# Optimization experiments

Measured on AMD Instinct MI355X. Metric: run time of the kernel, lower is better.

The kernel has to match this reference:

```python
import jax, jax.numpy as jnp
import numpy as np
import math

N = 8192
D_IN = 512
LOCAL_D = 512
GLOBAL_D = 512


def setup_inputs() -> dict:
    key = jax.random.key(0)
    ks = jax.random.split(key, 16)
    s = 1.0 / math.sqrt(D_IN)
    adj = jax.random.bernoulli(ks[0], 0.01, (N, N))
    adj = adj | jnp.eye(N, dtype=bool)
    return {
        "adj_matrix": adj,
        "x": jax.random.normal(ks[1], (N, D_IN), jnp.float32),
        "masked_x": jax.random.normal(ks[2], (N, D_IN), jnp.float32),
        # weights stored as [in, out] so y = x @ W (+ b)
        "Wlq": jax.random.normal(ks[3], (D_IN, LOCAL_D), jnp.float32) * s,
        "Wlk": jax.random.normal(ks[4], (D_IN, LOCAL_D), jnp.float32) * s,
        "Wlv": jax.random.normal(ks[5], (D_IN, D_IN), jnp.float32) * s,
        "blv": jax.random.normal(ks[6], (D_IN,), jnp.float32) * 0.01,
        "Wgq": jax.random.normal(ks[7], (D_IN, GLOBAL_D), jnp.float32) * s,
        "Wgk": jax.random.normal(ks[8], (D_IN, GLOBAL_D), jnp.float32) * s,
        "Wgv": jax.random.normal(ks[9], (D_IN, D_IN), jnp.float32) * s,
        "bgv": jax.random.normal(ks[10], (D_IN,), jnp.float32) * 0.01,
        "Wes": jax.random.normal(ks[11], (D_IN, 1), jnp.float32) * s,
        "Wev": jax.random.normal(ks[12], (D_IN, D_IN), jnp.float32) * s,
        "bev": jax.random.normal(ks[13], (D_IN,), jnp.float32) * 0.01,
    }


def reference(adj_matrix, x, masked_x, Wlq, Wlk, Wlv, blv, Wgq, Wgk, Wgv, bgv, Wes, Wev, bev):
    scale = 1.0 / math.sqrt(D_IN)  # note: original scales by sqrt(d_in), not sqrt(local_d)
    x_bar = jnp.mean(x, axis=0, keepdims=True)            # [1, d_in]

    lQ = masked_x @ Wlq                                   # [N, local_d]
    lK = x @ Wlk                                          # [N, local_d]
    lV = x @ Wlv + blv                                    # [N, d_out]
    gQ = masked_x @ Wgq                                   # [N, global_d]
    gK = x_bar @ Wgk                                      # [1, global_d]
    gV = x_bar @ Wgv + bgv                                # [1, d_out]
    es = masked_x @ Wes                                   # [N, 1]
    eV = masked_x @ Wev + bev                             # [N, d_out]

    local_scores = (lQ @ lK.T) * scale                    # [N, N]
    local_scores = jnp.where(adj_matrix, local_scores, jnp.float32(-1e9))
    global_scores = (gQ @ gK.T) * scale                   # [N, 1]

    # joint stable softmax across local row + global scalar + essential scalar
    max_score = jnp.maximum(jnp.max(local_scores, axis=1, keepdims=True),
                            jnp.maximum(global_scores, es))  # [N, 1]
    le = jnp.exp(local_scores - max_score)                # [N, N]
    ge = jnp.exp(global_scores - max_score)               # [N, 1]
    ee = jnp.exp(es - max_score)                          # [N, 1]
    denom = jnp.sum(le, axis=-1, keepdims=True) + ge + ee # [N, 1]

    res = (le / denom) @ lV + (ge / denom) * gV + (ee / denom) * eV  # [N, d_out]
    x_recon = jnp.maximum(res, masked_x)
    return x_recon
```

## Files before the change

kernel.cpp:

```cpp
#include <hip/hip_runtime.h>

typedef unsigned short u16;
typedef unsigned int   u32;
typedef unsigned char  u8;
typedef __attribute__((ext_vector_type(8))) short bf16x8;
typedef __attribute__((ext_vector_type(4))) float f32x4;

#define DEV __device__ __forceinline__

static constexpr float SCALE = 0.044194173824159216f;
static constexpr float MFIX  = 8.0f;

DEV u16 f2bf(float f) {
  u32 u = __float_as_uint(f);
  u32 r = (u + 0x7fffu + ((u >> 16) & 1u)) >> 16;
  return (u16)r;
}
DEV float bf2f(u16 v) { u32 u = (u32)v << 16; return __uint_as_float(u); }

DEV void gl_lds16(const void* g, void* l) {
  __builtin_amdgcn_global_load_lds(
      (__attribute__((address_space(1))) void*)(void*)g,
      (__attribute__((address_space(3))) void*)l, 16, 0, 0);
}

__global__ void k_convert(const float* __restrict__ x, const float* __restrict__ mx,
                          u16* __restrict__ xbf, u16* __restrict__ mxbf) {
  const u32 stride = gridDim.x * blockDim.x;
  for (u32 idx = blockIdx.x * blockDim.x + threadIdx.x; idx < 2u * 1048576u; idx += stride) {
    const u32 t = idx >> 20;
    const u32 i = idx & 1048575u;
    const float4 v = t ? ((const float4*)mx)[i] : ((const float4*)x)[i];
    ushort4 o;
    o.x = f2bf(v.x); o.y = f2bf(v.y); o.z = f2bf(v.z); o.w = f2bf(v.w);
    ((ushort4*)(t ? mxbf : xbf))[i] = o;
  }
}

struct WtransJobs { const float* src[4]; u16* dst[4]; };

__global__ void k_wtrans(WtransJobs jobs) {
  __shared__ float tile[32][33];
  const int j  = blockIdx.z;
  const float* src = jobs.src[j];
  u16* dst = jobs.dst[j];
  const int o0 = blockIdx.x * 32;
  const int k0 = blockIdx.y * 32;
  const int tx = threadIdx.x, ty = threadIdx.y;
#pragma unroll
  for (int yy = 0; yy < 4; ++yy)
    tile[ty + yy * 8][tx] = src[(size_t)(k0 + ty + yy * 8) * 512 + (o0 + tx)];
  __syncthreads();
#pragma unroll
  for (int yy = 0; yy < 4; ++yy)
    dst[(size_t)(o0 + ty + yy * 8) * 512 + (k0 + tx)] = f2bf(tile[tx][ty + yy * 8]);
}

__global__ void k_adjdetect(const u8* __restrict__ adj, u32* __restrict__ flag) {
  u32 cnt = 0;
  const u32 stride = gridDim.x * blockDim.x;
  for (u32 i = blockIdx.x * blockDim.x + threadIdx.x; i < (1u << 22); i += stride)
    if ((i & 3u) && adj[i]) cnt++;
#pragma unroll
  for (int m = 1; m <= 32; m <<= 1) cnt += __shfl_xor(cnt, m);
  if ((threadIdx.x & 63) == 0 && cnt) atomicAdd(flag, cnt);
}

__global__ void k_adjbits(const u8* __restrict__ adj, const u32* __restrict__ flag,
                          u32* __restrict__ adjb) {
  const int row = blockIdx.x;
  const int w = threadIdx.x;
  u32 res = 0;
  if (*flag > 100u) {
    const uint4* p = (const uint4*)(adj + (size_t)row * 8192 + w * 32);
#pragma unroll
    for (int i = 0; i < 2; ++i) {
      const uint4 q = p[i];
      const u32 vs[4] = {q.x, q.y, q.z, q.w};
#pragma unroll
      for (int jj = 0; jj < 4; ++jj) {
        const u32 v = vs[jj];
        const int base = i * 16 + jj * 4;
        res |= ((v & 0x000000FFu) ? 1u : 0u) << (base + 0);
        res |= ((v & 0x0000FF00u) ? 1u : 0u) << (base + 1);
        res |= ((v & 0x00FF0000u) ? 1u : 0u) << (base + 2);
        res |= ((v & 0xFF000000u) ? 1u : 0u) << (base + 3);
      }
    }
  } else {
    const uint4* p = (const uint4*)((const u32*)adj + (size_t)row * 8192 + w * 32);
#pragma unroll
    for (int i = 0; i < 8; ++i) {
      const uint4 q = p[i];
      res |= (q.x ? 1u : 0u) << (i * 4 + 0);
      res |= (q.y ? 1u : 0u) << (i * 4 + 1);
      res |= (q.z ? 1u : 0u) << (i * 4 + 2);
      res |= (q.w ? 1u : 0u) << (i * 4 + 3);
    }
  }
  adjb[(size_t)row * 256 + w] = res;
}

__global__ void k_colsum(const float* __restrict__ x, float* __restrict__ part) {
  const int c = threadIdx.x;
  const int b = blockIdx.x;
  const int r0 = b * 128;
  float s = 0.f;
  for (int r = 0; r < 128; ++r) s += x[(size_t)(r0 + r) * 512 + c];
  part[b * 512 + c] = s;
}

__global__ void k_colsum2(const float* __restrict__ part, float* __restrict__ xbar) {
  const int c = threadIdx.x;
  float s = 0.f;
  for (int b = 0; b < 64; ++b) s += part[b * 512 + c];
  xbar[c] = s * (1.0f / 8192.0f);
}

__global__ void k_gproj(const float* __restrict__ xbar, const float* __restrict__ Wgk,
                        const float* __restrict__ Wgv, const float* __restrict__ bgv,
                        float* __restrict__ gK, float* __restrict__ gV) {
  const int o = threadIdx.x;
  if (blockIdx.x == 0) {
    float s = 0.f;
    for (int k = 0; k < 512; ++k) s += xbar[k] * Wgk[(size_t)k * 512 + o];
    gK[o] = s;
  } else {
    float s = bgv[o];
    for (int k = 0; k < 512; ++k) s += xbar[k] * Wgv[(size_t)k * 512 + o];
    gV[o] = s;
  }
}

__global__ void k_wcomb(const float* __restrict__ Wgq, const float* __restrict__ gK,
                        float* __restrict__ wcomb) {
  const int w = threadIdx.x >> 6, l = threadIdx.x & 63;
  const int k = blockIdx.x * 4 + w;
  float s = 0.f;
  for (int o = l; o < 512; o += 64) s += Wgq[(size_t)k * 512 + o] * gK[o];
#pragma unroll
  for (int m = 1; m <= 32; m <<= 1) s += __shfl_xor(s, m);
  if (l == 0) wcomb[k] = s;
}

__global__ void k_esgsc(const float* __restrict__ mx, const float* __restrict__ Wes,
                        const float* __restrict__ wcomb, float* __restrict__ es,
                        float* __restrict__ gsc) {
  const int w = threadIdx.x >> 6, l = threadIdx.x & 63;
  const int row = blockIdx.x * 4 + w;
  float se = 0.f, sg = 0.f;
  for (int k = l; k < 512; k += 64) {
    const float v = mx[(size_t)row * 512 + k];
    se += v * Wes[k];
    sg += v * wcomb[k];
  }
#pragma unroll
  for (int m = 1; m <= 32; m <<= 1) { se += __shfl_xor(se, m); sg += __shfl_xor(sg, m); }
  if (l == 0) { es[row] = se; gsc[row] = sg * SCALE; }
}

struct GemmOuts { u16* obf[2]; float* of32[2]; const float* bias[2]; };

__global__ __launch_bounds__(256) void k_gemm(const u16* __restrict__ A,
                                              const u16* __restrict__ BT, GemmOuts outs) {
  __shared__ char lds[16384];
  char* ldsA = lds;
  char* ldsB = lds + 8192;
  const int tid = threadIdx.x;
  const int w = tid >> 6, l = tid & 63, g = l >> 4, ln = l & 15;
  const int wr = w >> 1, wc = w & 1;
  const int bm0 = blockIdx.x * 128, bn0 = blockIdx.y * 128;
  f32x4 acc[4][4] = {};
  for (int kt = 0; kt < 16; ++kt) {
    const int k0 = kt * 32;
    __syncthreads();
#pragma unroll
    for (int it = 0; it < 2; ++it) {
      const int i = it * 256 + tid;
      const int o = i * 16;
      const int row = o >> 6;
      const int pos = (o ^ (((o >> 7) & 3) << 4)) & 63;
      const int ldso = (it * 256 + w * 64) * 16;
      gl_lds16((const char*)A + ((size_t)(bm0 + row) * 512 + k0) * 2 + pos, ldsA + ldso);
      gl_lds16((const char*)BT + ((size_t)(bn0 + row) * 512 + k0) * 2 + pos, ldsB + ldso);
    }
    __syncthreads();
    bf16x8 a[4], b[4];
#pragma unroll
    for (int i = 0; i < 4; ++i) {
      const int r = wr * 64 + i * 16 + ln;
      int off = r * 64 + g * 16; off ^= ((r >> 1) & 3) << 4;
      a[i] = *(const bf16x8*)(ldsA + off);
    }
#pragma unroll
    for (int j = 0; j < 4; ++j) {
      const int r = wc * 64 + j * 16 + ln;
      int off = r * 64 + g * 16; off ^= ((r >> 1) & 3) << 4;
      b[j] = *(const bf16x8*)(ldsB + off);
    }
#pragma unroll
    for (int i = 0; i < 4; ++i)
#pragma unroll
      for (int j = 0; j < 4; ++j)
        acc[i][j] = __builtin_amdgcn_mfma_f32_16x16x32_bf16(a[i], b[j], acc[i][j], 0, 0, 0);
  }
#pragma unroll
  for (int j = 0; j < 4; ++j) {
    const int gcol = bn0 + wc * 64 + j * 16 + ln;
    const int seg = gcol >> 9, c = gcol & 511;
    const float bias = outs.bias[seg] ? outs.bias[seg][c] : 0.f;
#pragma unroll
    for (int i = 0; i < 4; ++i) {
#pragma unroll
      for (int r = 0; r < 4; ++r) {
        const int grow = bm0 + wr * 64 + i * 16 + g * 4 + r;
        const float v = acc[i][j][r] + bias;
        if (outs.of32[seg]) outs.of32[seg][(size_t)grow * 512 + c] = v;
        else                outs.obf[seg][(size_t)grow * 512 + c] = f2bf(v);
      }
    }
  }
}

__global__ void k_vtrans(const u16* __restrict__ lV, u16* __restrict__ lVT) {
  __shared__ u16 tile[32][33];
  const int c0 = blockIdx.x * 32;
  const int r0 = blockIdx.y * 32;
  const int tx = threadIdx.x, ty = threadIdx.y;
#pragma unroll
  for (int yy = 0; yy < 4; ++yy)
    tile[ty + yy * 8][tx] = lV[(size_t)(r0 + ty + yy * 8) * 512 + (c0 + tx)];
  __syncthreads();
#pragma unroll
  for (int yy = 0; yy < 4; ++yy)
    lVT[(size_t)(c0 + ty + yy * 8) * 8192 + (r0 + tx)] = tile[tx][ty + yy * 8];
}

__global__ __launch_bounds__(256, 2) void k_attn(
    const u16* __restrict__ lQ, const u16* __restrict__ lK, const u16* __restrict__ lVT,
    const u32* __restrict__ adjb, u16* __restrict__ Opart, float* __restrict__ lpart) {
  __shared__ char lds[69632];
  char* ldsK = lds;
  char* ldsVT = lds + 32768;
  const int tid = threadIdx.x;
  const int w = tid >> 6, l = tid & 63, g = l >> 4, ln = l & 15;
  const int qg = w >> 1, dh = w & 1;
  char* ldsP = lds + 65536 + qg * 1024;
  const int bid = blockIdx.x;
  const int split = (bid & 7) >> 1;
  const int rblk = ((bid >> 3) << 1) | (bid & 1);
  const int rbase = rblk * 32 + qg * 16;

  bf16x8 q[16];
#pragma unroll
  for (int kk = 0; kk < 16; ++kk)
    q[kk] = *(const bf16x8*)(lQ + (size_t)(rbase + ln) * 512 + kk * 32 + g * 8);

  f32x4 acc[16] = {};
  float rl = 0.f;

  for (int ct = 0; ct < 64; ++ct) {
    const int c0 = split * 2048 + ct * 32;
    __syncthreads();
#pragma unroll
    for (int it = 0; it < 8; ++it) {
      const int o = (it * 256 + tid) * 16;
      const int row = o >> 10;
      const int pos = (o ^ ((row & 7) << 4)) & 1023;
      gl_lds16((const char*)lK + (size_t)(c0 + row) * 1024 + pos,
               ldsK + (it * 256 + w * 64) * 16);
    }
#pragma unroll
    for (int it = 0; it < 8; ++it) {
      const int o = (it * 256 + tid) * 16;
      const int row = o >> 6;
      const int pos = (o ^ (((o >> 7) & 3) << 4)) & 63;
      gl_lds16((const char*)lVT + (size_t)row * 16384 + (size_t)c0 * 2 + pos,
               ldsVT + (it * 256 + w * 64) * 16);
    }
    __syncthreads();

    const u32 wd = adjb[(size_t)(rbase + ln) * 256 + (c0 >> 5)];

    f32x4 s = {};
    {
      const int ra = dh * 16 + ln;
      const int sw = (ra & 7) << 4;
      __builtin_amdgcn_s_setprio(1);
#pragma unroll
      for (int kk = 0; kk < 16; ++kk) {
        const int off = (ra * 1024 + kk * 64 + g * 16) ^ sw;
        const bf16x8 kf = *(const bf16x8*)(ldsK + off);
        s = __builtin_amdgcn_mfma_f32_16x16x32_bf16(kf, q[kk], s, 0, 0, 0);
      }
      __builtin_amdgcn_s_setprio(0);
    }

    float p[4];
#pragma unroll
    for (int r = 0; r < 4; ++r) {
      const int kc = dh * 16 + g * 4 + r;
      p[r] = ((wd >> kc) & 1) ? __expf(s[r] * SCALE - MFIX) : 0.f;
      rl += p[r];
    }

    {
      const int sw = ((ln >> 1) & 3) << 4;
      ushort4 w0;
      w0.x = f2bf(p[0]); w0.y = f2bf(p[1]); w0.z = f2bf(p[2]); w0.w = f2bf(p[3]);
      *(ushort4*)(ldsP + ((ln * 64 + dh * 32 + g * 8) ^ sw)) = w0;
    }
    __syncthreads();

    const bf16x8 pa = *(const bf16x8*)(ldsP + ((ln * 64 + g * 16) ^ (((ln >> 1) & 3) << 4)));
    __builtin_amdgcn_s_setprio(1);
#pragma unroll
    for (int t = 0; t < 16; ++t) {
      const int r = (dh * 16 + t) * 16 + ln;
      int off = r * 64 + g * 16; off ^= ((r >> 1) & 3) << 4;
      const bf16x8 vf = *(const bf16x8*)(ldsVT + off);
      acc[t] = __builtin_amdgcn_mfma_f32_16x16x32_bf16(pa, vf, acc[t], 0, 0, 0);
    }
    __builtin_amdgcn_s_setprio(0);
  }

#pragma unroll
  for (int t = 0; t < 16; ++t)
#pragma unroll
    for (int i = 0; i < 4; ++i)
      Opart[((size_t)split * 8192 + rbase + g * 4 + i) * 512 + dh * 256 + t * 16 + ln] =
          f2bf(acc[t][i]);
  rl += __shfl_xor(rl, 16);
  rl += __shfl_xor(rl, 32);
  if (l < 16) lpart[((size_t)split * 2 + dh) * 8192 + rbase + l] = rl;
}

__global__ void k_combine(const u16* __restrict__ Opart, const float* __restrict__ lpart,
                          const float* __restrict__ gsc, const float* __restrict__ es,
                          const float* __restrict__ gV, const float* __restrict__ eV,
                          const float* __restrict__ mx, float* __restrict__ out) {
  const int row = blockIdx.x;
  const int tid = threadIdx.x;
  const float gs = gsc[row], e = es[row];
  const float M = fmaxf(MFIX, fmaxf(gs, e));
  const float eg = __expf(gs - M), ee = __expf(e - M);
  const float fL = __expf(MFIX - M);
  float lsum = 0.f;
#pragma unroll
  for (int s = 0; s < 8; ++s) lsum += lpart[(size_t)s * 8192 + row];
  const float inv = 1.f / (eg + ee + fL * lsum);
  for (int d = tid; d < 512; d += 256) {
    float o = 0.f;
#pragma unroll
    for (int s = 0; s < 4; ++s)
      o += bf2f(Opart[((size_t)s * 8192 + row) * 512 + d]);
    o = o * fL + eg * gV[d] + ee * eV[(size_t)row * 512 + d];
    out[(size_t)row * 512 + d] = fmaxf(o * inv, mx[(size_t)row * 512 + d]);
  }
}

static constexpr size_t OFF_XBF   = 0;
static constexpr size_t OFF_MXBF  = OFF_XBF   + (size_t)8192 * 512 * 2;
static constexpr size_t OFF_WMT   = OFF_MXBF  + (size_t)8192 * 512 * 2;
static constexpr size_t OFF_WXT   = OFF_WMT   + (size_t)1024 * 512 * 2;
static constexpr size_t OFF_LQ    = OFF_WXT   + (size_t)1024 * 512 * 2;
static constexpr size_t OFF_LK    = OFF_LQ    + (size_t)8192 * 512 * 2;
static constexpr size_t OFF_LV    = OFF_LK    + (size_t)8192 * 512 * 2;
static constexpr size_t OFF_LVT   = OFF_LV    + (size_t)8192 * 512 * 2;
static constexpr size_t OFF_EV    = OFF_LVT   + (size_t)8192 * 512 * 2;
static constexpr size_t OFF_ADJB  = OFF_EV    + (size_t)8192 * 512 * 4;
static constexpr size_t OFF_COLP  = OFF_ADJB  + (size_t)8192 * 256 * 4;
static constexpr size_t OFF_XBAR  = OFF_COLP  + (size_t)64 * 512 * 4;
static constexpr size_t OFF_GK    = OFF_XBAR  + 2048;
static constexpr size_t OFF_GV    = OFF_GK    + 2048;
static constexpr size_t OFF_WCOMB = OFF_GV    + 2048;
static constexpr size_t OFF_ES    = OFF_WCOMB + 2048;
static constexpr size_t OFF_GSC   = OFF_ES    + (size_t)8192 * 4;
static constexpr size_t OFF_OPART = OFF_GSC   + (size_t)8192 * 4;
static constexpr size_t OFF_LPART = OFF_OPART + (size_t)4 * 8192 * 512 * 2;
static constexpr size_t OFF_FLAG  = OFF_LPART + (size_t)8 * 8192 * 4;
static constexpr size_t WS_NEEDED = OFF_FLAG  + 64;

extern "C" void kernel_launch(void* const* d_in, const int* in_sizes, int n_in,
                              void* d_out, int out_size, void* d_ws, size_t ws_size,
                              hipStream_t stream) {
  const u8*    adj = (const u8*)d_in[0];
  const float* x   = (const float*)d_in[1];
  const float* mx  = (const float*)d_in[2];
  const float* Wlq = (const float*)d_in[3];
  const float* Wlk = (const float*)d_in[4];
  const float* Wlv = (const float*)d_in[5];
  const float* blv = (const float*)d_in[6];
  const float* Wgq = (const float*)d_in[7];
  const float* Wgk = (const float*)d_in[8];
  const float* Wgv = (const float*)d_in[9];
  const float* bgv = (const float*)d_in[10];
  const float* Wes = (const float*)d_in[11];
  const float* Wev = (const float*)d_in[12];
  const float* bev = (const float*)d_in[13];
  float* out = (float*)d_out;

  if (ws_size < WS_NEEDED) return;

  char* ws = (char*)d_ws;
  u16*   x_bf   = (u16*)(ws + OFF_XBF);
  u16*   mx_bf  = (u16*)(ws + OFF_MXBF);
  u16*   WmT    = (u16*)(ws + OFF_WMT);
  u16*   WxT    = (u16*)(ws + OFF_WXT);
  u16*   lQ     = (u16*)(ws + OFF_LQ);
  u16*   lK     = (u16*)(ws + OFF_LK);
  u16*   lV     = (u16*)(ws + OFF_LV);
  u16*   lVT    = (u16*)(ws + OFF_LVT);
  float* eV     = (float*)(ws + OFF_EV);
  u32*   adjb   = (u32*)(ws + OFF_ADJB);
  float* colp   = (float*)(ws + OFF_COLP);
  float* xbar   = (float*)(ws + OFF_XBAR);
  float* gK     = (float*)(ws + OFF_GK);
  float* gV     = (float*)(ws + OFF_GV);
  float* wcomb  = (float*)(ws + OFF_WCOMB);
  float* es     = (float*)(ws + OFF_ES);
  float* gsc    = (float*)(ws + OFF_GSC);
  u16*   Opart  = (u16*)(ws + OFF_OPART);
  float* lpart  = (float*)(ws + OFF_LPART);
  u32*   flag   = (u32*)(ws + OFF_FLAG);

  hipMemsetAsync(flag, 0, 4, stream);
  k_adjdetect<<<1024, 256, 0, stream>>>(adj, flag);

  k_convert<<<2048, 256, 0, stream>>>(x, mx, x_bf, mx_bf);

  WtransJobs wj;
  wj.src[0] = Wlq; wj.dst[0] = WmT;
  wj.src[1] = Wev; wj.dst[1] = WmT + (size_t)512 * 512;
  wj.src[2] = Wlk; wj.dst[2] = WxT;
  wj.src[3] = Wlv; wj.dst[3] = WxT + (size_t)512 * 512;
  k_wtrans<<<dim3(16, 16, 4), dim3(32, 8), 0, stream>>>(wj);

  k_adjbits<<<8192, 256, 0, stream>>>(adj, flag, adjb);
  k_colsum<<<64, 512, 0, stream>>>(x, colp);
  k_colsum2<<<1, 512, 0, stream>>>(colp, xbar);
  k_gproj<<<2, 512, 0, stream>>>(xbar, Wgk, Wgv, bgv, gK, gV);
  k_wcomb<<<128, 256, 0, stream>>>(Wgq, gK, wcomb);
  k_esgsc<<<2048, 256, 0, stream>>>(mx, Wes, wcomb, es, gsc);

  GemmOuts o1;
  o1.obf[0] = lQ;      o1.of32[0] = nullptr; o1.bias[0] = nullptr;
  o1.obf[1] = nullptr; o1.of32[1] = eV;      o1.bias[1] = bev;
  k_gemm<<<dim3(64, 8), 256, 0, stream>>>(mx_bf, WmT, o1);

  GemmOuts o2;
  o2.obf[0] = lK; o2.of32[0] = nullptr; o2.bias[0] = nullptr;
  o2.obf[1] = lV; o2.of32[1] = nullptr; o2.bias[1] = blv;
  k_gemm<<<dim3(64, 8), 256, 0, stream>>>(x_bf, WxT, o2);

  k_vtrans<<<dim3(16, 256), dim3(32, 8), 0, stream>>>(lV, lVT);
  k_attn<<<dim3(1024), 256, 0, stream>>>(lQ, lK, lVT, adjb, Opart, lpart);
  k_combine<<<8192, 256, 0, stream>>>(Opart, lpart, gsc, es, gV, eV, mx, out);
}
```

Before: 453.9 us.

## Merge two projection GEMMs into one launch and share V fragments across query groups

The two projection GEMM launches are combined into one grid, with blockIdx.y selecting the job, so the launch gap goes away and the GPU stays fuller. In the attention kernel each wave now reads P for both 16-row query groups and computes 8 output column tiles for both, instead of 16 column tiles for one group. This halves the V-fragment LDS reads per MFMA. It costs an extra P read per wave and changes the accumulator layout and output indexing.

Result: no change. 455.0 us (+0.2%).

```diff
diff --git a/kernel.cpp b/kernel.cpp
--- a/kernel.cpp
+++ b/kernel.cpp
@@ -161,15 +161,21 @@
 
 struct GemmOuts { u16* obf[2]; float* of32[2]; const float* bias[2]; };
 
-__global__ __launch_bounds__(256) void k_gemm(const u16* __restrict__ A,
-                                              const u16* __restrict__ BT, GemmOuts outs) {
+__global__ __launch_bounds__(256) void k_gemm(const u16* __restrict__ A0,
+                                              const u16* __restrict__ BT0, GemmOuts o0j,
+                                              const u16* __restrict__ A1,
+                                              const u16* __restrict__ BT1, GemmOuts o1j) {
   __shared__ char lds[16384];
   char* ldsA = lds;
   char* ldsB = lds + 8192;
+  const int job = blockIdx.y >> 3;
+  const u16* A = job ? A1 : A0;
+  const u16* BT = job ? BT1 : BT0;
+  GemmOuts outs = job ? o1j : o0j;
   const int tid = threadIdx.x;
   const int w = tid >> 6, l = tid & 63, g = l >> 4, ln = l & 15;
   const int wr = w >> 1, wc = w & 1;
-  const int bm0 = blockIdx.x * 128, bn0 = blockIdx.y * 128;
+  const int bm0 = blockIdx.x * 128, bn0 = (blockIdx.y & 7) * 128;
   f32x4 acc[4][4] = {};
   for (int kt = 0; kt < 16; ++kt) {
     const int k0 = kt * 32;
@@ -245,7 +251,9 @@
   const int tid = threadIdx.x;
   const int w = tid >> 6, l = tid & 63, g = l >> 4, ln = l & 15;
   const int qg = w >> 1, dh = w & 1;
-  char* ldsP = lds + 65536 + qg * 1024;
+  char* ldsP0 = lds + 65536;
+  char* ldsP1 = lds + 66560;
+  char* ldsP = qg ? ldsP1 : ldsP0;
   const int bid = blockIdx.x;
   const int split = (bid & 7) >> 1;
   const int rblk = ((bid >> 3) << 1) | (bid & 1);
@@ -256,7 +264,7 @@
   for (int kk = 0; kk < 16; ++kk)
     q[kk] = *(const bf16x8*)(lQ + (size_t)(rbase + ln) * 512 + kk * 32 + g * 8);
 
-  f32x4 acc[16] = {};
+  f32x4 acc[2][8] = {};
   float rl = 0.f;
 
   for (int ct = 0; ct < 64; ++ct) {
@@ -312,24 +320,29 @@
     }
     __syncthreads();
 
-    const bf16x8 pa = *(const bf16x8*)(ldsP + ((ln * 64 + g * 16) ^ (((ln >> 1) & 3) << 4)));
+    const int psw = (ln * 64 + g * 16) ^ (((ln >> 1) & 3) << 4);
+    const bf16x8 pa0 = *(const bf16x8*)(ldsP0 + psw);
+    const bf16x8 pa1 = *(const bf16x8*)(ldsP1 + psw);
     __builtin_amdgcn_s_setprio(1);
 #pragma unroll
-    for (int t = 0; t < 16; ++t) {
-      const int r = (dh * 16 + t) * 16 + ln;
+    for (int t = 0; t < 8; ++t) {
+      const int r = (w * 8 + t) * 16 + ln;
       int off = r * 64 + g * 16; off ^= ((r >> 1) & 3) << 4;
       const bf16x8 vf = *(const bf16x8*)(ldsVT + off);
-      acc[t] = __builtin_amdgcn_mfma_f32_16x16x32_bf16(pa, vf, acc[t], 0, 0, 0);
+      acc[0][t] = __builtin_amdgcn_mfma_f32_16x16x32_bf16(pa0, vf, acc[0][t], 0, 0, 0);
+      acc[1][t] = __builtin_amdgcn_mfma_f32_16x16x32_bf16(pa1, vf, acc[1][t], 0, 0, 0);
     }
     __builtin_amdgcn_s_setprio(0);
   }
 
 #pragma unroll
-  for (int t = 0; t < 16; ++t)
-#pragma unroll
-    for (int i = 0; i < 4; ++i)
-      Opart[((size_t)split * 8192 + rbase + g * 4 + i) * 512 + dh * 256 + t * 16 + ln] =
-          f2bf(acc[t][i]);
+  for (int qq = 0; qq < 2; ++qq)
+#pragma unroll
+    for (int t = 0; t < 8; ++t)
+#pragma unroll
+      for (int i = 0; i < 4; ++i)
+        Opart[((size_t)split * 8192 + rblk * 32 + qq * 16 + g * 4 + i) * 512 +
+              w * 128 + t * 16 + ln] = f2bf(acc[qq][t][i]);
   rl += __shfl_xor(rl, 16);
   rl += __shfl_xor(rl, 32);
   if (l < 16) lpart[((size_t)split * 2 + dh) * 8192 + rbase + l] = rl;
@@ -446,12 +459,10 @@
   GemmOuts o1;
   o1.obf[0] = lQ;      o1.of32[0] = nullptr; o1.bias[0] = nullptr;
   o1.obf[1] = nullptr; o1.of32[1] = eV;      o1.bias[1] = bev;
-  k_gemm<<<dim3(64, 8), 256, 0, stream>>>(mx_bf, WmT, o1);
-
   GemmOuts o2;
   o2.obf[0] = lK; o2.of32[0] = nullptr; o2.bias[0] = nullptr;
   o2.obf[1] = lV; o2.of32[1] = nullptr; o2.bias[1] = blv;
-  k_gemm<<<dim3(64, 8), 256, 0, stream>>>(x_bf, WxT, o2);
+  k_gemm<<<dim3(64, 16), 256, 0, stream>>>(mx_bf, WmT, o1, x_bf, WxT, o2);
 
   k_vtrans<<<dim3(16, 256), dim3(32, 8), 0, stream>>>(lV, lVT);
   k_attn<<<dim3(1024), 256, 0, stream>>>(lQ, lK, lVT, adjb, Opart, lpart);
```
